# Kernel optimization log

Hardware: AMD Instinct MI355X
Metric: run time of the kernel (lower is better)

Reference implementation:

```python
import jax, jax.numpy as jnp
import numpy as np

B, TQ, TKV, D, H = 4, 512, 4096, 1024, 8
HEAD_DIM = D // H


def setup_inputs() -> dict:
    key = jax.random.key(0)
    ks = jax.random.split(key, 8)
    s = 0.02
    inputs_q = jax.random.normal(ks[0], (B, TQ, D), jnp.float32)
    inputs_kv = jax.random.normal(ks[1], (B, TKV, D), jnp.float32)
    attention_mask = jax.random.randint(ks[2], (B, TQ, TKV), 0, 2).astype(bool)
    Wq = jax.random.normal(ks[3], (D, D), jnp.float32) * s
    Wk = jax.random.normal(ks[4], (D, D), jnp.float32) * s
    Wv = jax.random.normal(ks[5], (D, D), jnp.float32) * s
    Wo = jax.random.normal(ks[6], (D, D), jnp.float32) * s
    zb = jnp.zeros((D,), jnp.float32)
    return {"inputs_q": inputs_q, "inputs_kv": inputs_kv, "attention_mask": attention_mask,
            "Wq": Wq, "bq": zb, "Wk": Wk, "bk": zb, "Wv": Wv, "bv": zb, "Wo": Wo, "bo": zb}


def _split_heads(x, h):
    b, t, c = x.shape
    return x.reshape(b, t, h, c // h).transpose(0, 2, 1, 3)  # b h t d


def reference(inputs_q, inputs_kv, attention_mask, Wq, bq, Wk, bk, Wv, bv, Wo, bo):
    q = _split_heads(inputs_q @ Wq + bq, H)   # [b,h,tq,d]
    k = _split_heads(inputs_kv @ Wk + bk, H)  # [b,h,tkv,d]
    v = _split_heads(inputs_kv @ Wv + bv, H)  # [b,h,tkv,d]
    scale = 1.0 / np.sqrt(HEAD_DIM).astype(np.float32)
    scores = jnp.einsum('bhtd,bhTd->bhtT', q, k) * scale
    large_k = jnp.asarray(1e30, scores.dtype)  # 1e30 for fp32 per source
    scores = jnp.where(attention_mask[:, None, :, :], scores, -large_k)
    probs = jax.nn.softmax(scores, axis=-1)
    summed = jnp.einsum('bhtT,bhTd->bhtd', probs, v)
    b, h, t, d = summed.shape
    summed = summed.transpose(0, 2, 1, 3).reshape(b, t, h * d)  # [b,tq,hiddens]
    # wipe rows whose mask is entirely zero (post-softmax wipe-masking)
    wipe = jnp.all(~attention_mask, axis=-1, keepdims=True)  # [b,tq,1]
    summed = jnp.where(wipe, jnp.zeros_like(summed), summed)
    return summed @ Wo + bo
```

## Files before the change

### kernel.cpp

```cpp
#include <hip/hip_runtime.h>
#include <cstdint>
#include <cstddef>

typedef unsigned short US;
typedef __bf16 bf16_t;
typedef bf16_t bf16x8 __attribute__((ext_vector_type(8)));
typedef float  f32x4  __attribute__((ext_vector_type(4)));
typedef US     us8    __attribute__((ext_vector_type(8)));
typedef US     us4    __attribute__((ext_vector_type(4)));

#define AS1 __attribute__((address_space(1)))
#define AS3 __attribute__((address_space(3)))

__device__ __forceinline__ void gl_lds16(const void* g, void* l) {
    __builtin_amdgcn_global_load_lds((AS1 unsigned int*)(size_t)g,
                                     (AS3 unsigned int*)l, 16, 0, 0);
}

__device__ __forceinline__ US f2bf(float f) {
    unsigned u = __builtin_bit_cast(unsigned, f);
    u += 0x7FFFu + ((u >> 16) & 1u);
    return (US)(u >> 16);
}

__device__ __forceinline__ float bf2f(US u) {
    return __builtin_bit_cast(float, (unsigned)u << 16);
}

__device__ __forceinline__ bf16x8 ldv8(const US* p) {
    return __builtin_bit_cast(bf16x8, *(const us8*)p);
}

__global__ void prep(const float* __restrict__ Xq, const float* __restrict__ Xkv,
                     const int* __restrict__ Mi, US* __restrict__ XqB,
                     US* __restrict__ XkvB, unsigned long long* __restrict__ MBits,
                     const float* __restrict__ Wq, const float* __restrict__ Wk,
                     const float* __restrict__ Wv, const float* __restrict__ Wo,
                     US* __restrict__ WTbase) {
    __shared__ float t[32][33];
    int b = blockIdx.x, tid = threadIdx.x;
    if (b < 2048) {
        int i = b * 256 + tid;
        float4 f = ((const float4*)Xq)[i];
        us4 o = { f2bf(f.x), f2bf(f.y), f2bf(f.z), f2bf(f.w) };
        ((us4*)XqB)[i] = o;
    } else if (b < 18432) {
        int i = (b - 2048) * 256 + tid;
        float4 f = ((const float4*)Xkv)[i];
        us4 o = { f2bf(f.x), f2bf(f.y), f2bf(f.z), f2bf(f.w) };
        ((us4*)XkvB)[i] = o;
    } else if (b < 51200) {
        int i = (b - 18432) * 256 + tid;
        int m = Mi[i];
        unsigned long long bits = __ballot(m != 0);
        if ((tid & 63) == 0) MBits[i >> 6] = bits;
    } else {
        int wb = b - 51200;
        int z = wb >> 10, rr = wb & 1023;
        int bx = rr & 31, by = rr >> 5;
        const float* W = (z == 0) ? Wq : (z == 1) ? Wk : (z == 2) ? Wv : Wo;
        US* WT = WTbase + (size_t)z * 1024 * 1024;
        int tx = tid & 31, ty = tid >> 5;
        int x = bx * 32 + tx;
#pragma unroll
        for (int r = 0; r < 4; ++r)
            t[ty + r * 8][tx] = W[(size_t)(by * 32 + ty + r * 8) * 1024 + x];
        __syncthreads();
        int nx = by * 32 + tx;
#pragma unroll
        for (int r = 0; r < 4; ++r)
            WT[(size_t)(bx * 32 + ty + r * 8) * 1024 + nx] = f2bf(t[tx][ty + r * 8]);
    }
}

template <int MODE, int BM>
__global__ __launch_bounds__(256, 2)
void gemm_bt(const US* __restrict__ A, const US* __restrict__ Bt,
             const float* __restrict__ bias, void* __restrict__ out,
             int tlog2, float scale) {
    constexpr int K = 1024, N = 1024, BK = 64;
    constexpr int MI = BM / 32;
    __shared__ US As[BM * BK];
    __shared__ US Bs[128 * BK];
    const int tid = threadIdx.x;
    const int wv = tid >> 6, ln = tid & 63;
    const int g = ln >> 4, c15 = ln & 15;
    const int m0 = blockIdx.x * BM, n0 = blockIdx.y * 128;
    const int wm = (wv & 1) * (BM / 2), wn = (wv >> 1) * 64;

    f32x4 acc[MI][4];
    const f32x4 z = {0.f, 0.f, 0.f, 0.f};
#pragma unroll
    for (int i = 0; i < MI; ++i)
#pragma unroll
        for (int j = 0; j < 4; ++j) acc[i][j] = z;

    const US* Ab = A + (size_t)m0 * K;
    const US* Bb = Bt + (size_t)n0 * K;

    for (int k0 = 0; k0 < K; k0 += BK) {
        __syncthreads();
#pragma unroll
        for (int q = 0; q < BM / 32; ++q) {
            int eb = (q * 256 + wv * 64) * 8;
            int r = (eb >> 6) + (ln >> 3);
            int sw = (ln & 7) ^ (r & 7);
            gl_lds16(Ab + (size_t)r * K + k0 + sw * 8, &As[eb]);
        }
#pragma unroll
        for (int q = 0; q < 4; ++q) {
            int eb = (q * 256 + wv * 64) * 8;
            int r = (eb >> 6) + (ln >> 3);
            int sw = (ln & 7) ^ (r & 7);
            gl_lds16(Bb + (size_t)r * K + k0 + sw * 8, &Bs[eb]);
        }
        __syncthreads();
#pragma unroll
        for (int ks = 0; ks < 2; ++ks) {
            bf16x8 a[MI], b[4];
#pragma unroll
            for (int i = 0; i < MI; ++i) {
                int p = (ks * 4 + g) ^ (c15 & 7);
                a[i] = ldv8(&As[(wm + i * 16 + c15) * BK + p * 8]);
            }
#pragma unroll
            for (int j = 0; j < 4; ++j) {
                int p = (ks * 4 + g) ^ (c15 & 7);
                b[j] = ldv8(&Bs[(wn + j * 16 + c15) * BK + p * 8]);
            }
#pragma unroll
            for (int i = 0; i < MI; ++i)
#pragma unroll
                for (int j = 0; j < 4; ++j)
                    acc[i][j] = __builtin_amdgcn_mfma_f32_16x16x32_bf16(a[i], b[j], acc[i][j], 0, 0, 0);
        }
    }

#pragma unroll
    for (int i = 0; i < MI; ++i) {
#pragma unroll
        for (int j = 0; j < 4; ++j) {
            int col = n0 + wn + j * 16 + c15;
            float bvv = bias[col];
#pragma unroll
            for (int r = 0; r < 4; ++r) {
                int row = m0 + wm + i * 16 + g * 4 + r;
                float v = (acc[i][j][r] + bvv) * scale;
                if (MODE == 0) {
                    int b_ = row >> tlog2;
                    int t = row & ((1 << tlog2) - 1);
                    int h = col >> 7, d = col & 127;
                    ((US*)out)[(((size_t)(b_ * 8 + h) << tlog2) + t) * 128 + d] = f2bf(v);
                } else {
                    ((float*)out)[(size_t)row * N + col] = v;
                }
            }
        }
    }
}

__global__ __launch_bounds__(256, 2)
void gemm_kv(const US* __restrict__ A, const US* __restrict__ BtK,
             const US* __restrict__ BtV, const float* __restrict__ bk,
             const float* __restrict__ bv, US* __restrict__ Kout,
             US* __restrict__ VTout) {
    constexpr int K = 1024, BK = 64;
    __shared__ US lds[3 * 128 * BK];
    US* As  = lds;
    US* BsK = lds + 128 * BK;
    US* BsV = lds + 2 * 128 * BK;
    const int tid = threadIdx.x;
    const int wv = tid >> 6, ln = tid & 63;
    const int g = ln >> 4, c15 = ln & 15;
    const int m0 = blockIdx.x * 128, n0 = blockIdx.y * 128;
    const int wm = (wv & 1) * 64, wn = (wv >> 1) * 64;

    f32x4 aK[4][4], aV[4][4];
    const f32x4 z = {0.f, 0.f, 0.f, 0.f};
#pragma unroll
    for (int i = 0; i < 4; ++i)
#pragma unroll
        for (int j = 0; j < 4; ++j) { aK[i][j] = z; aV[i][j] = z; }

    const US* Ab  = A   + (size_t)m0 * K;
    const US* BbK = BtK + (size_t)n0 * K;
    const US* BbV = BtV + (size_t)n0 * K;

    for (int k0 = 0; k0 < K; k0 += BK) {
        __syncthreads();
#pragma unroll
        for (int q = 0; q < 4; ++q) {
            int eb = (q * 256 + wv * 64) * 8;
            int r = (eb >> 6) + (ln >> 3);
            int sw = (ln & 7) ^ (r & 7);
            gl_lds16(Ab  + (size_t)r * K + k0 + sw * 8, &As[eb]);
            gl_lds16(BbK + (size_t)r * K + k0 + sw * 8, &BsK[eb]);
            gl_lds16(BbV + (size_t)r * K + k0 + sw * 8, &BsV[eb]);
        }
        __syncthreads();
#pragma unroll
        for (int ks = 0; ks < 2; ++ks) {
            bf16x8 a[4], bK[4], bV[4];
#pragma unroll
            for (int i = 0; i < 4; ++i) {
                int p = (ks * 4 + g) ^ (c15 & 7);
                a[i] = ldv8(&As[(wm + i * 16 + c15) * BK + p * 8]);
            }
#pragma unroll
            for (int j = 0; j < 4; ++j) {
                int p = (ks * 4 + g) ^ (c15 & 7);
                bK[j] = ldv8(&BsK[(wn + j * 16 + c15) * BK + p * 8]);
                bV[j] = ldv8(&BsV[(wn + j * 16 + c15) * BK + p * 8]);
            }
#pragma unroll
            for (int i = 0; i < 4; ++i)
#pragma unroll
                for (int j = 0; j < 4; ++j) {
                    aK[i][j] = __builtin_amdgcn_mfma_f32_16x16x32_bf16(a[i], bK[j], aK[i][j], 0, 0, 0);
                    aV[i][j] = __builtin_amdgcn_mfma_f32_16x16x32_bf16(a[i], bV[j], aV[i][j], 0, 0, 0);
                }
        }
    }

    const int h = n0 >> 7;
    const int b_ = m0 >> 12, tbase = m0 & 4095;

#pragma unroll
    for (int i = 0; i < 4; ++i) {
#pragma unroll
        for (int j = 0; j < 4; ++j) {
            int col = n0 + wn + j * 16 + c15;
            float bkv = bk[col];
            int d = col & 127;
#pragma unroll
            for (int r = 0; r < 4; ++r) {
                int row = m0 + wm + i * 16 + g * 4 + r;
                int t = row & 4095;
                Kout[(((size_t)(b_ * 8 + h) << 12) + t) * 128 + d] = f2bf(aK[i][j][r] + bkv);
            }
        }
    }

    __syncthreads();
    US* T = lds;
#pragma unroll
    for (int i = 0; i < 4; ++i) {
#pragma unroll
        for (int j = 0; j < 4; ++j) {
            int dcol = wn + j * 16 + c15;
            float bvv = bv[n0 + dcol];
#pragma unroll
            for (int r = 0; r < 4; ++r) {
                int kvrow = wm + i * 16 + g * 4 + r;
                T[dcol * 136 + kvrow] = f2bf(aV[i][j][r] + bvv);
            }
        }
    }
    __syncthreads();
    {
        int d = tid >> 1, half = (tid & 1) * 64;
        US* vrow = VTout + ((size_t)(b_ * 8 + h) * 128 + d) * 4096 + tbase + half;
        const US* tr = &T[d * 136 + half];
#pragma unroll
        for (int s = 0; s < 8; ++s)
            *(us8*)(vrow + s * 8) = *(const us8*)(tr + s * 8);
    }
}

__global__ __launch_bounds__(256, 3)
void flash(const US* __restrict__ Qh, const US* __restrict__ Kh,
           const US* __restrict__ VTh, const unsigned long long* __restrict__ MBits,
           US* __restrict__ Opart, float* __restrict__ Lpart) {
    __shared__ US Ks[64 * 128];
    __shared__ US Vs[128 * 64];
    __shared__ US Ps[4][32 * 64];
    const int tid = threadIdx.x, wv = tid >> 6, ln = tid & 63;
    const int g = ln >> 4, c15 = ln & 15;
    const int bid = blockIdx.x;
    const int qt = bid / 192;
    const int rest = bid - qt * 192;
    const int bh = rest / 6, sp = rest - bh * 6;
    const int qbase = qt * 128;
    const int b_ = bh >> 3;
    const int t0 = (sp < 4) ? sp * 11 : 44 + (sp - 4) * 10;
    const int nt = (sp < 4) ? 11 : 10;
    const int wq = wv * 32;

    bf16x8 qa[2][4];
#pragma unroll
    for (int ib = 0; ib < 2; ++ib) {
        const US* qrow = Qh + ((size_t)bh * 512 + qbase + wq + ib * 16 + c15) * 128;
#pragma unroll
        for (int ks = 0; ks < 4; ++ks)
            qa[ib][ks] = ldv8(qrow + ks * 32 + g * 8);
    }

    f32x4 o[8][2];
    const f32x4 z = {0.f, 0.f, 0.f, 0.f};
#pragma unroll
    for (int d = 0; d < 8; ++d) { o[d][0] = z; o[d][1] = z; }
    float l2[2] = {0.f, 0.f};

    const unsigned long long* Mrow[2];
    Mrow[0] = MBits + (size_t)(b_ * 512 + qbase + wq + c15) * 64;
    Mrow[1] = Mrow[0] + (size_t)16 * 64;
    const US* Kbase = Kh + ((size_t)bh * 4096 + (size_t)t0 * 64) * 128;
    const US* Vbase = VTh + (size_t)bh * 128 * 4096;
    US* Pw = &Ps[wv][0];

    for (int t = 0; t < nt; ++t) {
        int kv0 = (t0 + t) * 64;
        __syncthreads();
        const US* Kb = Kbase + (size_t)t * 64 * 128;
#pragma unroll
        for (int q = 0; q < 4; ++q) {
            int eb = (q * 256 + wv * 64) * 8;
            int r = (eb >> 7) + (ln >> 4);
            int sw = (ln & 15) ^ (r & 15);
            gl_lds16(Kb + (size_t)r * 128 + sw * 8, &Ks[eb]);
        }
#pragma unroll
        for (int q = 0; q < 4; ++q) {
            int eb = (q * 256 + wv * 64) * 8;
            int r = (eb >> 6) + (ln >> 3);
            int sw = (ln & 7) ^ (r & 7);
            gl_lds16(Vbase + (size_t)r * 4096 + kv0 + sw * 8, &Vs[eb]);
        }
        unsigned long long m64[2];
        m64[0] = Mrow[0][t0 + t];
        m64[1] = Mrow[1][t0 + t];
        __syncthreads();

#pragma unroll
        for (int kb = 0; kb < 4; ++kb) {
            f32x4 s0 = z, s1 = z;
#pragma unroll
            for (int ks = 0; ks < 4; ++ks) {
                bf16x8 kf = ldv8(&Ks[(kb * 16 + c15) * 128 + (((ks * 4 + g) ^ c15) * 8)]);
                s0 = __builtin_amdgcn_mfma_f32_16x16x32_bf16(kf, qa[0][ks], s0, 0, 0, 0);
                s1 = __builtin_amdgcn_mfma_f32_16x16x32_bf16(kf, qa[1][ks], s1, 0, 0, 0);
            }
            int cw = kb * 4 + g;
#pragma unroll
            for (int ib = 0; ib < 2; ++ib) {
                f32x4 sv = ib ? s1 : s0;
                unsigned mq = (unsigned)(m64[ib] >> (kb * 16 + g * 4)) & 15u;
                float p0 = (mq & 1u) ? __expf(sv[0]) : 0.f;
                float p1 = (mq & 2u) ? __expf(sv[1]) : 0.f;
                float p2 = (mq & 4u) ? __expf(sv[2]) : 0.f;
                float p3 = (mq & 8u) ? __expf(sv[3]) : 0.f;
                l2[ib] += (p0 + p1) + (p2 + p3);
                int q = ib * 16 + c15;
                US* wp = Pw + q * 64 + (((cw >> 1) ^ (q & 7)) * 8) + (cw & 1) * 4;
                us4 pv = { f2bf(p0), f2bf(p1), f2bf(p2), f2bf(p3) };
                *(us4*)wp = pv;
            }
        }

#pragma unroll
        for (int ks = 0; ks < 2; ++ks) {
            bf16x8 pf[2];
#pragma unroll
            for (int ib = 0; ib < 2; ++ib) {
                int q = ib * 16 + c15;
                pf[ib] = ldv8(&Pw[q * 64 + (((ks * 4 + g) ^ (q & 7)) * 8)]);
            }
#pragma unroll
            for (int d = 0; d < 8; ++d) {
                bf16x8 vf = ldv8(&Vs[(d * 16 + c15) * 64 + (((ks * 4 + g) ^ (c15 & 7)) * 8)]);
                o[d][0] = __builtin_amdgcn_mfma_f32_16x16x32_bf16(vf, pf[0], o[d][0], 0, 0, 0);
                o[d][1] = __builtin_amdgcn_mfma_f32_16x16x32_bf16(vf, pf[1], o[d][1], 0, 0, 0);
            }
        }
    }

    float lf[2];
#pragma unroll
    for (int ib = 0; ib < 2; ++ib) {
        float l = l2[ib];
        l += __shfl_xor(l, 16); l += __shfl_xor(l, 32);
        lf[ib] = l;
    }
    if (ln < 16) {
        size_t lb = ((size_t)sp * 32 + bh) * 512 + qbase + wq + c15;
        Lpart[lb] = lf[0];
        Lpart[lb + 16] = lf[1];
    }
    US* Ob = Opart + (((size_t)sp * 32 + bh) * 128 + g * 4) * 512 + qbase + wq + c15;
#pragma unroll
    for (int d = 0; d < 8; ++d)
#pragma unroll
        for (int r = 0; r < 4; ++r) {
            Ob[(size_t)(d * 16 + r) * 512] = f2bf(o[d][0][r]);
            Ob[(size_t)(d * 16 + r) * 512 + 16] = f2bf(o[d][1][r]);
        }
}

__global__ void combine(const US* __restrict__ Opart, const float* __restrict__ Lpart,
                        US* __restrict__ AO) {
    __shared__ float linv[128];
    __shared__ float T[128 * 33];
    const int qt = blockIdx.x, bh = blockIdx.y;
    const int b_ = bh >> 3, h = bh & 7;
    const int tid = threadIdx.x;
    const size_t spstride = (size_t)32 * 128 * 512;

    if (tid < 128) {
        float s = 0.f;
#pragma unroll
        for (int sp = 0; sp < 6; ++sp)
            s += Lpart[((size_t)sp * 32 + bh) * 512 + qt * 128 + tid];
        linv[tid] = (s > 0.f) ? 1.f / s : 0.f;
    }
    __syncthreads();

    for (int ds0 = 0; ds0 < 128; ds0 += 32) {
        if (ds0) __syncthreads();
        {
            int d = ds0 + (tid >> 3);
            int q0 = (tid & 7) * 16;
            const US* base = Opart + ((size_t)bh * 128 + d) * 512 + qt * 128 + q0;
            float acc[16];
#pragma unroll
            for (int i = 0; i < 16; ++i) acc[i] = 0.f;
#pragma unroll
            for (int sp = 0; sp < 6; ++sp) {
                us8 a = *(const us8*)(base + sp * spstride);
                us8 b = *(const us8*)(base + sp * spstride + 8);
#pragma unroll
                for (int i = 0; i < 8; ++i) {
                    acc[i] += bf2f(a[i]);
                    acc[8 + i] += bf2f(b[i]);
                }
            }
            int dd = d - ds0;
#pragma unroll
            for (int i = 0; i < 16; ++i)
                T[(q0 + i) * 33 + dd] = acc[i] * linv[q0 + i];
        }
        __syncthreads();
#pragma unroll
        for (int it = 0; it < 4; ++it) {
            int idx = tid + it * 256;
            int q = idx >> 3, c = idx & 7;
            const float* tr = &T[q * 33 + c * 4];
            us4 ov = { f2bf(tr[0]), f2bf(tr[1]), f2bf(tr[2]), f2bf(tr[3]) };
            *(us4*)(AO + ((size_t)(b_ * 512 + qt * 128 + q)) * 1024 + h * 128 + ds0 + c * 4) = ov;
        }
    }
}

extern "C" void kernel_launch(void* const* d_in, const int* in_sizes, int n_in,
                              void* d_out, int out_size, void* d_ws, size_t ws_size,
                              hipStream_t stream) {
    (void)in_sizes; (void)n_in; (void)out_size; (void)ws_size;
    const float* Xq  = (const float*)d_in[0];
    const float* Xkv = (const float*)d_in[1];
    const int*   Mi  = (const int*)d_in[2];
    const float* Wq  = (const float*)d_in[3];
    const float* bq  = (const float*)d_in[4];
    const float* Wk  = (const float*)d_in[5];
    const float* bk  = (const float*)d_in[6];
    const float* Wv  = (const float*)d_in[7];
    const float* bv  = (const float*)d_in[8];
    const float* Wo  = (const float*)d_in[9];
    const float* bo  = (const float*)d_in[10];
    float* out = (float*)d_out;

    char* p = (char*)d_ws;
    US* WT   = (US*)p; p += (size_t)4 * 1024 * 1024 * 2;
    US* AO   = (US*)p; p += (size_t)2048 * 1024 * 2;
    US* XqB  = (US*)p; p += (size_t)2048 * 1024 * 2;
    US* Qh   = (US*)p; p += (size_t)2048 * 1024 * 2;
    US* Kh   = (US*)p; p += (size_t)16384 * 1024 * 2;
    US* VTh  = (US*)p; p += (size_t)16384 * 1024 * 2;
    US* XkvB = (US*)p; p += (size_t)16384 * 1024 * 2;
    unsigned long long* MBits = (unsigned long long*)p; p += (size_t)131072 * 8;
    US* Opart    = XkvB;
    float* Lpart = (float*)XqB;

    prep<<<55296, 256, 0, stream>>>(Xq, Xkv, Mi, XqB, XkvB, MBits, Wq, Wk, Wv, Wo, WT);

    gemm_bt<0, 64><<<dim3(32, 8), 256, 0, stream>>>(XqB, WT, bq, Qh, 9, 0.08838834764831843f);
    gemm_kv<<<dim3(128, 8), 256, 0, stream>>>(XkvB, WT + 1048576, WT + 2097152,
                                              bk, bv, Kh, VTh);
    flash<<<768, 256, 0, stream>>>(Qh, Kh, VTh, MBits, Opart, Lpart);
    combine<<<dim3(4, 32), 256, 0, stream>>>(Opart, Lpart, AO);
    gemm_bt<1, 64><<<dim3(32, 8), 256, 0, stream>>>(AO, WT + 3145728, bo, out, 0, 1.0f);
}
```

Measured before the change: 344.1 us.

## Merge Q/KV projections and mask packing into one kernel, shrink prep grid

Prep now uses a fixed 4096-block grid with a grid-stride loop for the bf16 conversions plus one weight-transpose tile per block, and no longer packs the mask. A new combined kernel interleaves mask bit-packing blocks, the Q projection blocks and the fused K/V projection blocks in a 7-slot pattern. The goal is to cut launch count and let the small Q GEMM and the memory-bound mask packing overlap with the large KV GEMM rather than run as separate serial launches. In exchange, heterogeneous blocks now share one launch-bounds and LDS allocation, and wave scheduling becomes less uniform.

```diff
diff --git a/kernel.cpp b/kernel.cpp
--- a/kernel.cpp
+++ b/kernel.cpp
@@ -32,31 +32,29 @@
 }
 
 __global__ void prep(const float* __restrict__ Xq, const float* __restrict__ Xkv,
-                     const int* __restrict__ Mi, US* __restrict__ XqB,
-                     US* __restrict__ XkvB, unsigned long long* __restrict__ MBits,
+                     US* __restrict__ XqB, US* __restrict__ XkvB,
                      const float* __restrict__ Wq, const float* __restrict__ Wk,
                      const float* __restrict__ Wv, const float* __restrict__ Wo,
                      US* __restrict__ WTbase) {
     __shared__ float t[32][33];
-    int b = blockIdx.x, tid = threadIdx.x;
-    if (b < 2048) {
-        int i = b * 256 + tid;
-        float4 f = ((const float4*)Xq)[i];
-        us4 o = { f2bf(f.x), f2bf(f.y), f2bf(f.z), f2bf(f.w) };
-        ((us4*)XqB)[i] = o;
-    } else if (b < 18432) {
-        int i = (b - 2048) * 256 + tid;
-        float4 f = ((const float4*)Xkv)[i];
-        us4 o = { f2bf(f.x), f2bf(f.y), f2bf(f.z), f2bf(f.w) };
-        ((us4*)XkvB)[i] = o;
-    } else if (b < 51200) {
-        int i = (b - 18432) * 256 + tid;
-        int m = Mi[i];
-        unsigned long long bits = __ballot(m != 0);
-        if ((tid & 63) == 0) MBits[i >> 6] = bits;
-    } else {
-        int wb = b - 51200;
-        int z = wb >> 10, rr = wb & 1023;
+    const int b = blockIdx.x, tid = threadIdx.x;
+
+    for (int u = b; u < 18432; u += 4096) {
+        if (u < 2048) {
+            int i = u * 256 + tid;
+            float4 f = ((const float4*)Xq)[i];
+            us4 o = { f2bf(f.x), f2bf(f.y), f2bf(f.z), f2bf(f.w) };
+            ((us4*)XqB)[i] = o;
+        } else {
+            int i = (u - 2048) * 256 + tid;
+            float4 f = ((const float4*)Xkv)[i];
+            us4 o = { f2bf(f.x), f2bf(f.y), f2bf(f.z), f2bf(f.w) };
+            ((us4*)XkvB)[i] = o;
+        }
+    }
+
+    {
+        int z = b >> 10, rr = b & 1023;
         int bx = rr & 31, by = rr >> 5;
         const float* W = (z == 0) ? Wq : (z == 1) ? Wk : (z == 2) ? Wv : Wo;
         US* WT = WTbase + (size_t)z * 1024 * 1024;
@@ -73,118 +71,119 @@
     }
 }
 
-template <int MODE, int BM>
 __global__ __launch_bounds__(256, 2)
-void gemm_bt(const US* __restrict__ A, const US* __restrict__ Bt,
-             const float* __restrict__ bias, void* __restrict__ out,
-             int tlog2, float scale) {
-    constexpr int K = 1024, N = 1024, BK = 64;
-    constexpr int MI = BM / 32;
-    __shared__ US As[BM * BK];
-    __shared__ US Bs[128 * BK];
+void mid(const US* __restrict__ XkvB, const US* __restrict__ XqB,
+         const US* __restrict__ WT, const float* __restrict__ bq,
+         const float* __restrict__ bk, const float* __restrict__ bv,
+         const int* __restrict__ Mi, unsigned long long* __restrict__ MBits,
+         US* __restrict__ Qh, US* __restrict__ Kout, US* __restrict__ VTout) {
+    __shared__ US lds[3 * 128 * 64];
+    const int bid = blockIdx.x;
+    const int grp = bid / 7, res = bid % 7;
     const int tid = threadIdx.x;
     const int wv = tid >> 6, ln = tid & 63;
     const int g = ln >> 4, c15 = ln & 15;
-    const int m0 = blockIdx.x * BM, n0 = blockIdx.y * 128;
-    const int wm = (wv & 1) * (BM / 2), wn = (wv >> 1) * 64;
-
-    f32x4 acc[MI][4];
+    constexpr int K = 1024, BK = 64;
     const f32x4 z = {0.f, 0.f, 0.f, 0.f};
-#pragma unroll
-    for (int i = 0; i < MI; ++i)
-#pragma unroll
-        for (int j = 0; j < 4; ++j) acc[i][j] = z;
-
-    const US* Ab = A + (size_t)m0 * K;
-    const US* Bb = Bt + (size_t)n0 * K;
-
-    for (int k0 = 0; k0 < K; k0 += BK) {
-        __syncthreads();
-#pragma unroll
-        for (int q = 0; q < BM / 32; ++q) {
-            int eb = (q * 256 + wv * 64) * 8;
-            int r = (eb >> 6) + (ln >> 3);
-            int sw = (ln & 7) ^ (r & 7);
-            gl_lds16(Ab + (size_t)r * K + k0 + sw * 8, &As[eb]);
-        }
-#pragma unroll
-        for (int q = 0; q < 4; ++q) {
-            int eb = (q * 256 + wv * 64) * 8;
-            int r = (eb >> 6) + (ln >> 3);
-            int sw = (ln & 7) ^ (r & 7);
-            gl_lds16(Bb + (size_t)r * K + k0 + sw * 8, &Bs[eb]);
-        }
-        __syncthreads();
-#pragma unroll
-        for (int ks = 0; ks < 2; ++ks) {
-            bf16x8 a[MI], b[4];
-#pragma unroll
-            for (int i = 0; i < MI; ++i) {
-                int p = (ks * 4 + g) ^ (c15 & 7);
-                a[i] = ldv8(&As[(wm + i * 16 + c15) * BK + p * 8]);
-            }
+
+    if (res == 2 || res == 6) {
+        int idx = grp * 2 + (res == 6);
+#pragma unroll 4
+        for (int it = 0; it < 64; ++it) {
+            int i = idx * 16384 + it * 256 + tid;
+            int m = Mi[i];
+            unsigned long long bits = __ballot(m != 0);
+            if ((tid & 63) == 0) MBits[i >> 6] = bits;
+        }
+        return;
+    }
+
+    if (res == 5) {
+        int idx = grp;
+        const int m0 = (idx & 31) * 64, n0 = (idx >> 5) * 128;
+        const int wm = (wv & 1) * 32, wn = (wv >> 1) * 64;
+        US* As = lds;
+        US* Bs = lds + 64 * 64;
+        f32x4 acc[2][4];
+#pragma unroll
+        for (int i = 0; i < 2; ++i)
+#pragma unroll
+            for (int j = 0; j < 4; ++j) acc[i][j] = z;
+        const US* Ab = XqB + (size_t)m0 * K;
+        const US* Bb = WT + (size_t)n0 * K;
+        for (int k0 = 0; k0 < K; k0 += BK) {
+            __syncthreads();
+#pragma unroll
+            for (int q = 0; q < 2; ++q) {
+                int eb = (q * 256 + wv * 64) * 8;
+                int r = (eb >> 6) + (ln >> 3);
+                int sw = (ln & 7) ^ (r & 7);
+                gl_lds16(Ab + (size_t)r * K + k0 + sw * 8, &As[eb]);
+            }
+#pragma unroll
+            for (int q = 0; q < 4; ++q) {
+                int eb = (q * 256 + wv * 64) * 8;
+                int r = (eb >> 6) + (ln >> 3);
+                int sw = (ln & 7) ^ (r & 7);
+                gl_lds16(Bb + (size_t)r * K + k0 + sw * 8, &Bs[eb]);
+            }
+            __syncthreads();
+#pragma unroll
+            for (int ks = 0; ks < 2; ++ks) {
+                bf16x8 a[2], b[4];
+#pragma unroll
+                for (int i = 0; i < 2; ++i) {
+                    int p = (ks * 4 + g) ^ (c15 & 7);
+                    a[i] = ldv8(&As[(wm + i * 16 + c15) * BK + p * 8]);
+                }
+#pragma unroll
+                for (int j = 0; j < 4; ++j) {
+                    int p = (ks * 4 + g) ^ (c15 & 7);
+                    b[j] = ldv8(&Bs[(wn + j * 16 + c15) * BK + p * 8]);
+                }
+#pragma unroll
+                for (int i = 0; i < 2; ++i)
+#pragma unroll
+                    for (int j = 0; j < 4; ++j)
+                        acc[i][j] = __builtin_amdgcn_mfma_f32_16x16x32_bf16(a[i], b[j], acc[i][j], 0, 0, 0);
+            }
+        }
+        const float scale = 0.08838834764831843f;
+#pragma unroll
+        for (int i = 0; i < 2; ++i) {
 #pragma unroll
             for (int j = 0; j < 4; ++j) {
-                int p = (ks * 4 + g) ^ (c15 & 7);
-                b[j] = ldv8(&Bs[(wn + j * 16 + c15) * BK + p * 8]);
-            }
-#pragma unroll
-            for (int i = 0; i < MI; ++i)
-#pragma unroll
-                for (int j = 0; j < 4; ++j)
-                    acc[i][j] = __builtin_amdgcn_mfma_f32_16x16x32_bf16(a[i], b[j], acc[i][j], 0, 0, 0);
-        }
-    }
-
-#pragma unroll
-    for (int i = 0; i < MI; ++i) {
-#pragma unroll
-        for (int j = 0; j < 4; ++j) {
-            int col = n0 + wn + j * 16 + c15;
-            float bvv = bias[col];
-#pragma unroll
-            for (int r = 0; r < 4; ++r) {
-                int row = m0 + wm + i * 16 + g * 4 + r;
-                float v = (acc[i][j][r] + bvv) * scale;
-                if (MODE == 0) {
-                    int b_ = row >> tlog2;
-                    int t = row & ((1 << tlog2) - 1);
-                    int h = col >> 7, d = col & 127;
-                    ((US*)out)[(((size_t)(b_ * 8 + h) << tlog2) + t) * 128 + d] = f2bf(v);
-                } else {
-                    ((float*)out)[(size_t)row * N + col] = v;
+                int col = n0 + wn + j * 16 + c15;
+                float bvv = bq[col];
+                int h = col >> 7, d = col & 127;
+#pragma unroll
+                for (int r = 0; r < 4; ++r) {
+                    int row = m0 + wm + i * 16 + g * 4 + r;
+                    int b_ = row >> 9, tq = row & 511;
+                    Qh[(((size_t)(b_ * 8 + h) << 9) + tq) * 128 + d] =
+                        f2bf((acc[i][j][r] + bvv) * scale);
                 }
             }
         }
-    }
-}
-
-__global__ __launch_bounds__(256, 2)
-void gemm_kv(const US* __restrict__ A, const US* __restrict__ BtK,
-             const US* __restrict__ BtV, const float* __restrict__ bk,
-             const float* __restrict__ bv, US* __restrict__ Kout,
-             US* __restrict__ VTout) {
-    constexpr int K = 1024, BK = 64;
-    __shared__ US lds[3 * 128 * BK];
+        return;
+    }
+
+    int idx = grp * 4 + res - (res > 2);
+    const int m0 = (idx & 127) * 128, n0 = (idx >> 7) * 128;
+    const int wm = (wv & 1) * 64, wn = (wv >> 1) * 64;
     US* As  = lds;
     US* BsK = lds + 128 * BK;
     US* BsV = lds + 2 * 128 * BK;
-    const int tid = threadIdx.x;
-    const int wv = tid >> 6, ln = tid & 63;
-    const int g = ln >> 4, c15 = ln & 15;
-    const int m0 = blockIdx.x * 128, n0 = blockIdx.y * 128;
-    const int wm = (wv & 1) * 64, wn = (wv >> 1) * 64;
 
     f32x4 aK[4][4], aV[4][4];
-    const f32x4 z = {0.f, 0.f, 0.f, 0.f};
 #pragma unroll
     for (int i = 0; i < 4; ++i)
 #pragma unroll
         for (int j = 0; j < 4; ++j) { aK[i][j] = z; aV[i][j] = z; }
 
-    const US* Ab  = A   + (size_t)m0 * K;
-    const US* BbK = BtK + (size_t)n0 * K;
-    const US* BbV = BtV + (size_t)n0 * K;
+    const US* Ab  = XkvB + (size_t)m0 * K;
+    const US* BbK = WT + 1048576 + (size_t)n0 * K;
+    const US* BbV = WT + 2097152 + (size_t)n0 * K;
 
     for (int k0 = 0; k0 < K; k0 += BK) {
         __syncthreads();
@@ -265,6 +264,80 @@
         for (int s = 0; s < 8; ++s)
             *(us8*)(vrow + s * 8) = *(const us8*)(tr + s * 8);
     }
+}
+
+__global__ __launch_bounds__(256, 2)
+void gemm_o(const US* __restrict__ A, const US* __restrict__ Bt,
+            const float* __restrict__ bias, float* __restrict__ out) {
+    constexpr int K = 1024, N = 1024, BK = 64, BM = 64;
+    __shared__ US As[BM * BK];
+    __shared__ US Bs[128 * BK];
+    const int tid = threadIdx.x;
+    const int wv = tid >> 6, ln = tid & 63;
+    const int g = ln >> 4, c15 = ln & 15;
+    const int m0 = blockIdx.x * BM, n0 = blockIdx.y * 128;
+    const int wm = (wv & 1) * 32, wn = (wv >> 1) * 64;
+
+    f32x4 acc[2][4];
+    const f32x4 z = {0.f, 0.f, 0.f, 0.f};
+#pragma unroll
+    for (int i = 0; i < 2; ++i)
+#pragma unroll
+        for (int j = 0; j < 4; ++j) acc[i][j] = z;
+
+    const US* Ab = A + (size_t)m0 * K;
+    const US* Bb = Bt + (size_t)n0 * K;
+
+    for (int k0 = 0; k0 < K; k0 += BK) {
+        __syncthreads();
+#pragma unroll
+        for (int q = 0; q < 2; ++q) {
+            int eb = (q * 256 + wv * 64) * 8;
+            int r = (eb >> 6) + (ln >> 3);
+            int sw = (ln & 7) ^ (r & 7);
+            gl_lds16(Ab + (size_t)r * K + k0 + sw * 8, &As[eb]);
+        }
+#pragma unroll
+        for (int q = 0; q < 4; ++q) {
+            int eb = (q * 256 + wv * 64) * 8;
+            int r = (eb >> 6) + (ln >> 3);
+            int sw = (ln & 7) ^ (r & 7);
+            gl_lds16(Bb + (size_t)r * K + k0 + sw * 8, &Bs[eb]);
+        }
+        __syncthreads();
+#pragma unroll
+        for (int ks = 0; ks < 2; ++ks) {
+            bf16x8 a[2], b[4];
+#pragma unroll
+            for (int i = 0; i < 2; ++i) {
+                int p = (ks * 4 + g) ^ (c15 & 7);
+                a[i] = ldv8(&As[(wm + i * 16 + c15) * BK + p * 8]);
+            }
+#pragma unroll
+            for (int j = 0; j < 4; ++j) {
+                int p = (ks * 4 + g) ^ (c15 & 7);
+                b[j] = ldv8(&Bs[(wn + j * 16 + c15) * BK + p * 8]);
+            }
+#pragma unroll
+            for (int i = 0; i < 2; ++i)
+#pragma unroll
+                for (int j = 0; j < 4; ++j)
+                    acc[i][j] = __builtin_amdgcn_mfma_f32_16x16x32_bf16(a[i], b[j], acc[i][j], 0, 0, 0);
+        }
+    }
+
+#pragma unroll
+    for (int i = 0; i < 2; ++i)
+#pragma unroll
+        for (int j = 0; j < 4; ++j) {
+            int col = n0 + wn + j * 16 + c15;
+            float bvv = bias[col];
+#pragma unroll
+            for (int r = 0; r < 4; ++r) {
+                int row = m0 + wm + i * 16 + g * 4 + r;
+                out[(size_t)row * N + col] = acc[i][j][r] + bvv;
+            }
+        }
 }
 
 __global__ __launch_bounds__(256, 3)
@@ -479,12 +552,9 @@
     US* Opart    = XkvB;
     float* Lpart = (float*)XqB;
 
-    prep<<<55296, 256, 0, stream>>>(Xq, Xkv, Mi, XqB, XkvB, MBits, Wq, Wk, Wv, Wo, WT);
-
-    gemm_bt<0, 64><<<dim3(32, 8), 256, 0, stream>>>(XqB, WT, bq, Qh, 9, 0.08838834764831843f);
-    gemm_kv<<<dim3(128, 8), 256, 0, stream>>>(XkvB, WT + 1048576, WT + 2097152,
-                                              bk, bv, Kh, VTh);
+    prep<<<4096, 256, 0, stream>>>(Xq, Xkv, XqB, XkvB, Wq, Wk, Wv, Wo, WT);
+    mid<<<1792, 256, 0, stream>>>(XkvB, XqB, WT, bq, bk, bv, Mi, MBits, Qh, Kh, VTh);
     flash<<<768, 256, 0, stream>>>(Qh, Kh, VTh, MBits, Opart, Lpart);
     combine<<<dim3(4, 32), 256, 0, stream>>>(Opart, Lpart, AO);
-    gemm_bt<1, 64><<<dim3(32, 8), 256, 0, stream>>>(AO, WT + 3145728, bo, out, 0, 1.0f);
-}
+    gemm_o<<<dim3(32, 8), 256, 0, stream>>>(AO, WT + 3145728, bo, out);
+}
```

Result: slower. 368.3 us (+7.0%).
